# Optimization experiments

Measured on AMD Instinct MI355X. Metric: run time of the kernel, lower is better.

The kernel has to match this reference:

```python
import jax, jax.numpy as jnp
import numpy as np

L, B, DM, H, HID, NSPK, NB, NC, WIN = 128, 64, 1024, 256, 256, 2, 30, 6, 10
F = 2 * H            # biLSTM output feature dim
MEM = F + HID        # concat of node features and graph-conv output
R = 2 * NSPK * NSPK  # number of edge relations


def _build_edges():
    src_l, dst_l = [], []
    for j in range(L):
        for k in range(max(0, j - WIN), min(L, j + WIN + 1)):
            dst_l.append(j); src_l.append(k)
    dst = np.asarray(dst_l, np.int32); src = np.asarray(src_l, np.int32)
    offs = (np.arange(B, dtype=np.int32) * L)[:, None]
    edge_dst = (dst[None] + offs).reshape(-1)
    edge_src = (src[None] + offs).reshape(-1)
    mask = np.zeros((L, L), bool); mask[dst, src] = True
    return edge_src, edge_dst, mask


def setup_inputs():
    key = jax.random.key(0)
    ks = iter(jax.random.split(key, 32))
    rn = lambda *s: jax.random.normal(next(ks), s, jnp.float32) * 0.05
    edge_src, edge_dst, edge_mask = _build_edges()
    return {
        'U': jax.random.normal(next(ks), (L, B, DM), jnp.float32),
        'umask': jnp.ones((B, L), jnp.float32),
        'Wih0': rn(2, 4 * H, DM), 'Whh0': rn(2, 4 * H, H), 'b0': rn(2, 4 * H),
        'Wih1': rn(2, 4 * H, F), 'Whh1': rn(2, 4 * H, H), 'b1': rn(2, 4 * H),
        'W_scalar': rn(F, L),
        'basis': rn(NB, F, HID), 'comp': rn(R, NB),
        'W_root': rn(F, HID), 'b_rgcn': rn(HID),
        'gc_W1': rn(HID, HID), 'gc_W2': rn(HID, HID), 'gc_b': rn(HID),
        'Wm': rn(MEM, MEM), 'bm': rn(MEM),
        'Wl': rn(MEM, HID), 'bl': rn(HID),
        'Ws': rn(HID, NC), 'bs': rn(NC),
        'speakers': jax.random.randint(next(ks), (L, B), 0, NSPK, jnp.int32),
        'edge_src': jnp.asarray(edge_src), 'edge_dst': jnp.asarray(edge_dst),
        'edge_mask': jnp.asarray(edge_mask),
    }


def _lstm_dir(x, Wih, Whh, b, reverse):
    Bx, Hh = x.shape[1], Whh.shape[1]
    def step(carry, xt):
        h, c = carry
        g = xt @ Wih.T + h @ Whh.T + b          # PyTorch gate order i,f,g,o
        i, f, gg, o = jnp.split(g, 4, axis=-1)
        c = jax.nn.sigmoid(f) * c + jax.nn.sigmoid(i) * jnp.tanh(gg)
        h = jax.nn.sigmoid(o) * jnp.tanh(c)
        return (h, c), h
    init = (jnp.zeros((Bx, Hh), x.dtype), jnp.zeros((Bx, Hh), x.dtype))
    return jax.lax.scan(step, init, x, reverse=reverse)[1]


def _bilstm(x, Wih, Whh, b):
    return jnp.concatenate([_lstm_dir(x, Wih[0], Whh[0], b[0], False),
                            _lstm_dir(x, Wih[1], Whh[1], b[1], True)], -1)


def reference(U, umask, Wih0, Whh0, b0, Wih1, Whh1, b1, W_scalar, basis, comp,
              W_root, b_rgcn, gc_W1, gc_W2, gc_b, Wm, bm, Wl, bl, Ws, bs,
              speakers, edge_src, edge_dst, edge_mask):
    # --- 2-layer biLSTM encoder ---
    feats = _bilstm(_bilstm(U, Wih0, Whh0, b0), Wih1, Whh1, b1)   # (L,B,F)
    # --- MaskedEdgeAttention ('attn1'): edge weights ---
    scale = jnp.einsum('sbd,dm->sbm', feats, W_scalar)            # (L,B,L)
    alpha = jax.nn.softmax(scale, axis=0).transpose(1, 2, 0)      # (B,Lt,Ls)
    masked = alpha * jnp.where(edge_mask, 1.0, 1e-10)
    scores = masked / masked.sum(-1, keepdims=True) * edge_mask
    b_idx = edge_dst // L; i0 = edge_dst % L; i1 = edge_src % L
    edge_norm = scores[b_idx, i0, i1]                             # (E,)
    # --- edge types: speaker pair + temporal direction ---
    s_dst = speakers[i0, b_idx]; s_src = speakers[i1, b_idx]
    e_dir = jnp.where(i0 < i1, 0, 1)
    edge_type = s_dst * (2 * NSPK) + s_src * 2 + e_dir            # (E,) in [0,R)
    # --- node features, conversation-major ---
    x = feats.transpose(1, 0, 2).reshape(B * L, F)                # (N,F)
    N = B * L
    # --- RGCNConv with basis decomposition ---
    W_rel = jnp.einsum('rb,bfo->rfo', comp, basis)                # (R,F,HID)
    x_rel = jnp.einsum('nf,rfo->nro', x, W_rel)                   # (N,R,HID)
    msg = x_rel[edge_src, edge_type] * edge_norm[:, None]
    h = jax.ops.segment_sum(msg, edge_dst, num_segments=N) + x @ W_root + b_rgcn
    # --- GraphConv ---
    agg = jax.ops.segment_sum(h[edge_src], edge_dst, num_segments=N)
    h2 = h @ gc_W1 + gc_b + agg @ gc_W2                           # (N,HID)
    em = jnp.concatenate([x, h2], -1)                             # (N,MEM)
    em = em.reshape(B, L, MEM).transpose(1, 0, 2)                 # (L,B,MEM)
    # --- MatchingAttention ('general2') at every timestep, vectorized ---
    um = umask.T                                                  # (L,B)
    x_tr = em @ Wm + bm                                           # (L,B,MEM)
    logits = jnp.einsum('tbm,sbm->tbs', x_tr, em * um[:, :, None]) * umask[None]
    a = jax.nn.softmax(jnp.tanh(logits), axis=2) * umask[None]
    a = a / a.sum(2, keepdims=True)
    att = jnp.einsum('tbs,sbm->tbm', a, em)
    hidden = jax.nn.relu(att @ Wl + bl)                           # dropout = eval identity
    logp = jax.nn.log_softmax(hidden @ Ws + bs, axis=2)           # (L,B,NC)
    return logp.transpose(1, 0, 2).reshape(B * L, NC)
```

## Files before the change

### kernel.cpp

```cpp
#include <hip/hip_runtime.h>
#include <cstdint>


typedef __attribute__((ext_vector_type(8))) short bf16x8;
typedef __attribute__((ext_vector_type(4))) float f32x4;

template<bool HASBIAS, bool ACCUM, bool RELU, bool OUTBF>
__global__ __launch_bounds__(256) void gemm_bf16_nt(
    const ushort* __restrict__ A, const ushort* __restrict__ Bt,
    const float* __restrict__ bias, void* __restrict__ Cv,
    int M, int N, int K, long sA, long sB, long sC, long sBias)
{
  const int bz = blockIdx.z;
  A += (long)bz * sA;
  Bt += (long)bz * sB;
  if (HASBIAS) bias += (long)bz * sBias;
  float*  Cf = OUTBF ? nullptr : ((float*)Cv + (long)bz * sC);
  ushort* Cb = OUTBF ? ((ushort*)Cv + (long)bz * sC) : nullptr;

  const int bn = blockIdx.x * 128, bm = blockIdx.y * 128;

  __shared__ ushort As[128][40];
  __shared__ ushort Bs[128][40];

  const int tid = threadIdx.x;
  const int wave = tid >> 6, lane = tid & 63;
  const int wm = (wave >> 1) * 64, wn = (wave & 1) * 64;
  const int fr = lane & 15;
  const int fk = (lane >> 4) * 8;

  f32x4 acc[4][4];
#pragma unroll
  for (int i = 0; i < 4; ++i)
#pragma unroll
    for (int j = 0; j < 4; ++j) acc[i][j] = (f32x4){0.f, 0.f, 0.f, 0.f};

  const int sr = tid >> 1;
  const int sq = (tid & 1) * 16;

  for (int k0 = 0; k0 < K; k0 += 32) {
    const uint4* ga = (const uint4*)(A + (long)(bm + sr) * K + k0 + sq);
    uint4 av0 = ga[0], av1 = ga[1];
    const uint4* gb = (const uint4*)(Bt + (long)(bn + sr) * K + k0 + sq);
    uint4 bv0 = gb[0], bv1 = gb[1];
    *(uint4*)&As[sr][sq] = av0;
    *(uint4*)&As[sr][sq + 8] = av1;
    *(uint4*)&Bs[sr][sq] = bv0;
    *(uint4*)&Bs[sr][sq + 8] = bv1;
    __syncthreads();

    bf16x8 af[4], bfr[4];
#pragma unroll
    for (int f = 0; f < 4; ++f) {
      af[f]  = *(const bf16x8*)&As[wm + f * 16 + fr][fk];
      bfr[f] = *(const bf16x8*)&Bs[wn + f * 16 + fr][fk];
    }
#pragma unroll
    for (int mf = 0; mf < 4; ++mf)
#pragma unroll
      for (int nf = 0; nf < 4; ++nf)
        acc[mf][nf] = __builtin_amdgcn_mfma_f32_16x16x32_bf16(
            af[mf], bfr[nf], acc[mf][nf], 0, 0, 0);
    __syncthreads();
  }

  float bv[4];
#pragma unroll
  for (int nf = 0; nf < 4; ++nf)
    bv[nf] = HASBIAS ? bias[bn + wn + nf * 16 + fr] : 0.f;

  const int crow0 = (lane >> 4) * 4;
#pragma unroll
  for (int mf = 0; mf < 4; ++mf)
#pragma unroll
    for (int r = 0; r < 4; ++r) {
      const long roff = (long)(bm + wm + mf * 16 + crow0 + r) * N + bn + wn;
#pragma unroll
      for (int nf = 0; nf < 4; ++nf) {
        float v = acc[mf][nf][r] + bv[nf];
        if (OUTBF) {
          unsigned u = __float_as_uint(v);
          u += 0x7fffu + ((u >> 16) & 1u);
          Cb[roff + nf * 16 + fr] = (ushort)(u >> 16);
        } else {
          if (ACCUM) v += Cf[roff + nf * 16 + fr];
          if (RELU) v = fmaxf(v, 0.f);
          Cf[roff + nf * 16 + fr] = v;
        }
      }
    }
}

__device__ __forceinline__ unsigned short f2bf(float f) {
  unsigned u = __float_as_uint(f);
  u += 0x7fffu + ((u >> 16) & 1u);
  return (unsigned short)(u >> 16);
}
__device__ __forceinline__ float fast_sig(float x) {
  return __builtin_amdgcn_rcpf(1.f + __expf(-x));
}
__device__ __forceinline__ float fast_tanh(float x) {
  const float xc = fminf(fmaxf(x, -15.f), 15.f);
  const float t = __expf(2.f * xc);
  return (t - 1.f) * __builtin_amdgcn_rcpf(t + 1.f);
}

__device__ __forceinline__ int sdot4_(uint a, uint b, int c) {
#if __has_builtin(__builtin_amdgcn_sdot4)
  return __builtin_amdgcn_sdot4((int)a, (int)b, c, false);
#else
  int r = c;
  r += ((int)(a << 24) >> 24) * ((int)(b << 24) >> 24);
  r += ((int)(a << 16) >> 24) * ((int)(b << 16) >> 24);
  r += ((int)(a << 8)  >> 24) * ((int)(b << 8)  >> 24);
  r += ((int)a >> 24)         * ((int)b >> 24);
  return r;
#endif
}

__global__ __launch_bounds__(256) void cvt_bf16_k(const float* __restrict__ src,
                                                  ushort* __restrict__ dst) {
  const long i = ((long)blockIdx.x * 256 + threadIdx.x) * 4;
  float4 v = *(const float4*)(src + i);
  ushort4 o;
  o.x = f2bf(v.x); o.y = f2bf(v.y); o.z = f2bf(v.z); o.w = f2bf(v.w);
  *(ushort4*)(dst + i) = o;
}

__global__ __launch_bounds__(256) void tp_bf16_k(const float* __restrict__ src,
                                                 ushort* __restrict__ dst,
                                                 int R, int C) {
  __shared__ float tile[32][33];
  const int c0 = blockIdx.x * 32, r0 = blockIdx.y * 32;
  const int tx = threadIdx.x & 31, ty = threadIdx.x >> 5;
#pragma unroll
  for (int j = 0; j < 4; ++j)
    tile[ty + j * 8][tx] = src[(long)(r0 + ty + j * 8) * C + c0 + tx];
  __syncthreads();
#pragma unroll
  for (int j = 0; j < 4; ++j)
    dst[(long)(c0 + ty + j * 8) * R + r0 + tx] = f2bf(tile[tx][ty + j * 8]);
}

__global__ __launch_bounds__(256) void emt_k(const ushort* __restrict__ src,
                                             ushort* __restrict__ dst) {
  __shared__ ushort tile[32][33];
  const int c0 = blockIdx.x * 32;
  const int r0 = blockIdx.y * 32;
  const int b = blockIdx.z;
  const ushort* s = src + (long)b * 98304;
  ushort* d = dst + (long)b * 98304;
  const int tx = threadIdx.x & 31, ty = threadIdx.x >> 5;
#pragma unroll
  for (int j = 0; j < 4; ++j)
    tile[ty + j * 8][tx] = s[(long)(r0 + ty + j * 8) * 768 + c0 + tx];
  __syncthreads();
#pragma unroll
  for (int j = 0; j < 4; ++j)
    d[(long)(c0 + ty + j * 8) * 128 + r0 + tx] = tile[tx][ty + j * 8];
}

__global__ __launch_bounds__(256) void pack_whh_i8_k(const float* __restrict__ Whh,
                                                     uint* __restrict__ Wq,
                                                     float* __restrict__ fscale) {
  const int wid = (blockIdx.x * 256 + threadIdx.x) >> 6;
  const int lane = threadIdx.x & 63;
  const int d = wid >> 10, gi = wid & 1023;
  const float* row = Whh + ((long)d * 1024 + gi) * 256 + lane * 4;
  float v0 = row[0], v1 = row[1], v2 = row[2], v3 = row[3];
  float am = fmaxf(fmaxf(fabsf(v0), fabsf(v1)), fmaxf(fabsf(v2), fabsf(v3)));
#pragma unroll
  for (int off = 32; off > 0; off >>= 1) am = fmaxf(am, __shfl_xor(am, off, 64));
  am = fmaxf(am, 1e-12f);
  const float inv = 127.f / am;
  int q0 = __float2int_rn(v0 * inv), q1 = __float2int_rn(v1 * inv);
  int q2 = __float2int_rn(v2 * inv), q3 = __float2int_rn(v3 * inv);
  uint w = (uint)(q0 & 255) | ((uint)(q1 & 255) << 8) |
           ((uint)(q2 & 255) << 16) | ((uint)(q3 & 255) << 24);
  Wq[((long)d * 64 + lane) * 1024 + gi] = w;
  if (lane == 0) fscale[d * 1024 + gi] = am / 127.f;
}

__global__ __launch_bounds__(1024) void lstm4_k(
    const float* __restrict__ Xg,
    const uint* __restrict__ Wq,
    const float* __restrict__ fscale,
    ushort* __restrict__ out)
{
  const int bx = blockIdx.x;
  const int d = bx >> 6, b = bx & 63;
  const int tid = threadIdx.x;

  __shared__ uint hq[2][64];
  __shared__ float preactF[1024];

  uint w[64];
  const uint* wrow = Wq + (long)d * 65536 + tid;
#pragma unroll
  for (int k4 = 0; k4 < 64; ++k4) w[k4] = wrow[k4 * 1024];

  if (tid < 128) ((uint*)hq)[tid] = 0u;

  const float fsc = fscale[d * 1024 + tid] * (1.0f / 127.0f);
  const float* Xd = Xg + (long)d * 8192 * 1024;

  float c = 0.f;
  float x0 = 0.f, x1 = 0.f, x2 = 0.f, x3 = 0.f;
  if (tid < 256) {
    const float* xr = Xd + ((long)((d ? 127 : 0) * 64 + b)) * 1024;
    x0 = xr[tid]; x1 = xr[tid + 256]; x2 = xr[tid + 512]; x3 = xr[tid + 768];
  }
  __syncthreads();

  int cur = 0;
  for (int step = 0; step < 128; ++step) {
    const int t = d ? 127 - step : step;

    float n0 = 0.f, n1 = 0.f, n2 = 0.f, n3 = 0.f;
    if (tid < 256 && step + 1 < 128) {
      const float* xr = Xd + ((long)((d ? 126 - step : step + 1) * 64 + b)) * 1024;
      n0 = xr[tid]; n1 = xr[tid + 256]; n2 = xr[tid + 512]; n3 = xr[tid + 768];
    }

    int acc = 0;
    const uint4* hrow = (const uint4*)hq[cur];
#pragma unroll
    for (int k16 = 0; k16 < 16; ++k16) {
      uint4 h4 = hrow[k16];
      acc = sdot4_(w[k16 * 4 + 0], h4.x, acc);
      acc = sdot4_(w[k16 * 4 + 1], h4.y, acc);
      acc = sdot4_(w[k16 * 4 + 2], h4.z, acc);
      acc = sdot4_(w[k16 * 4 + 3], h4.w, acc);
    }
    preactF[tid] = (float)acc * fsc;
    __syncthreads();

    if (tid < 256) {
      float p0 = x0 + preactF[tid];
      float p1 = x1 + preactF[tid + 256];
      float p2 = x2 + preactF[tid + 512];
      float p3 = x3 + preactF[tid + 768];
      const float ig = fast_sig(p0), fg = fast_sig(p1);
      const float gg = fast_tanh(p2), og = fast_sig(p3);
      c = fg * c + ig * gg;
      const float h = og * fast_tanh(c);
      out[((long)(t * 64 + b)) * 512 + (d << 8) + tid] = f2bf(h);
      ((char*)hq[cur ^ 1])[tid] = (char)__float2int_rn(h * 127.f);
      x0 = n0; x1 = n1; x2 = n2; x3 = n3;
    }
    __syncthreads();
    cur ^= 1;
  }
}

__global__ __launch_bounds__(128) void edge_softmax_k(const float* __restrict__ scale,
                                                      float* __restrict__ scores) {
  const int bx = blockIdx.x;
  const int b = bx >> 7, t = bx & 127;
  const int s = threadIdx.x;
  __shared__ float red[128];
  const float v = scale[((long)(s * 64 + b)) * 128 + t];
  red[s] = v; __syncthreads();
  for (int off = 64; off > 0; off >>= 1) { if (s < off) red[s] = fmaxf(red[s], red[s + off]); __syncthreads(); }
  const float m = red[0]; __syncthreads();
  const float e = expf(v - m);
  red[s] = e; __syncthreads();
  for (int off = 64; off > 0; off >>= 1) { if (s < off) red[s] += red[s + off]; __syncthreads(); }
  const float esum = red[0]; __syncthreads();
  const float alpha = e / esum;
  const int dd = s - t;
  const bool inwin = (dd <= 10) && (dd >= -10);
  const float masked = alpha * (inwin ? 1.0f : 1e-10f);
  red[s] = masked; __syncthreads();
  for (int off = 64; off > 0; off >>= 1) { if (s < off) red[s] += red[s + off]; __syncthreads(); }
  const float msum = red[0];
  scores[(long)bx * 128 + s] = inwin ? (masked / msum) : 0.f;
}

__global__ __launch_bounds__(256) void xbuf_k(const ushort* __restrict__ featsbf,
                                              ushort* __restrict__ xbf) {
  const int n = blockIdx.x;
  const int b = n >> 7, t = n & 127;
  const int tid = threadIdx.x;
  const ushort* src = featsbf + (long)(t * 64 + b) * 512;
  ushort* dst = xbf + (long)n * 512;
  dst[tid] = src[tid];
  dst[tid + 256] = src[tid + 256];
}

__global__ __launch_bounds__(256) void wrel_k(const float* __restrict__ basis,
                                              const float* __restrict__ comp,
                                              ushort* __restrict__ wrel2t) {
  const int f = blockIdx.x;
  const int o = threadIdx.x;
  __shared__ float cs[240];
  if (o < 240) cs[o] = comp[o];
  __syncthreads();
  float acc[8];
#pragma unroll
  for (int r = 0; r < 8; ++r) acc[r] = 0.f;
  for (int bb = 0; bb < 30; ++bb) {
    const float v = basis[((long)bb * 512 + f) * 256 + o];
#pragma unroll
    for (int r = 0; r < 8; ++r) acc[r] = fmaf(cs[r * 30 + bb], v, acc[r]);
  }
#pragma unroll
  for (int r = 0; r < 8; ++r)
    wrel2t[((long)(r * 256 + o)) * 512 + f] = f2bf(acc[r]);
}

__global__ __launch_bounds__(256) void rgcn_gather_k(
    const float* __restrict__ xrel, const float* __restrict__ scores,
    const float* __restrict__ hroot, const int* __restrict__ spk,
    float* __restrict__ h, ushort* __restrict__ hbf)
{
  const int n = blockIdx.x;
  const int b = n >> 7, t = n & 127;
  const int o = threadIdx.x;
  const int lo = max(t - 10, 0), hi = min(t + 10, 127);
  const int cnt = hi - lo + 1;
  __shared__ int spks[21];
  __shared__ float wv[21];
  __shared__ int spkt_s;
  if (o < cnt) {
    spks[o] = spk[(lo + o) * 64 + b];
    wv[o] = scores[((long)(b * 128 + t)) * 128 + lo + o];
  }
  if (o == 0) spkt_s = spk[t * 64 + b];
  __syncthreads();
  const int spkt = spkt_s;
  float acc = hroot[(long)n * 256 + o];
  for (int q = 0; q < cnt; ++q) {
    const int s = lo + q;
    const int et = spkt * 4 + spks[q] * 2 + ((t < s) ? 0 : 1);
    acc = fmaf(xrel[(((long)(b * 128 + s)) * 8 + et) * 256 + o], wv[q], acc);
  }
  h[(long)n * 256 + o] = acc;
  hbf[(long)n * 256 + o] = f2bf(acc);
}

__global__ __launch_bounds__(256) void agg_k(const float* __restrict__ h,
                                             ushort* __restrict__ aggbf) {
  const int n = blockIdx.x;
  const int b = n >> 7, t = n & 127;
  const int o = threadIdx.x;
  const int lo = max(t - 10, 0), hi = min(t + 10, 127);
  float acc = 0.f;
  for (int s = lo; s <= hi; ++s) acc += h[((long)(b * 128 + s)) * 256 + o];
  aggbf[(long)n * 256 + o] = f2bf(acc);
}

__global__ __launch_bounds__(256) void em_k(const ushort* __restrict__ xbf,
                                            const float* __restrict__ h2,
                                            ushort* __restrict__ embf) {
  const int n = blockIdx.x;
  const int tid = threadIdx.x;
  embf[(long)n * 768 + tid] = xbf[(long)n * 512 + tid];
  embf[(long)n * 768 + 256 + tid] = xbf[(long)n * 512 + 256 + tid];
  embf[(long)n * 768 + 512 + tid] = f2bf(h2[(long)n * 256 + tid]);
}

__global__ __launch_bounds__(128) void match_softmax_k(const float* __restrict__ logits,
                                                       const float* __restrict__ umask,
                                                       ushort* __restrict__ abf) {
  const int bx = blockIdx.x;
  const int b = bx >> 7;
  const int s = threadIdx.x;
  __shared__ float red[128];
  const float* row = logits + (long)bx * 128;
  const float um = umask[b * 128 + s];
  const float v = tanhf(row[s] * um * um);
  red[s] = v; __syncthreads();
  for (int off = 64; off > 0; off >>= 1) { if (s < off) red[s] = fmaxf(red[s], red[s + off]); __syncthreads(); }
  const float m = red[0]; __syncthreads();
  const float e = expf(v - m);
  red[s] = e; __syncthreads();
  for (int off = 64; off > 0; off >>= 1) { if (s < off) red[s] += red[s + off]; __syncthreads(); }
  const float es = red[0]; __syncthreads();
  const float p = (e / es) * um;
  red[s] = p; __syncthreads();
  for (int off = 64; off > 0; off >>= 1) { if (s < off) red[s] += red[s + off]; __syncthreads(); }
  const float ps = red[0];
  abf[(long)bx * 128 + s] = f2bf(p / ps);
}

__global__ __launch_bounds__(256) void final_k(const float* __restrict__ hidden,
                                               const float* __restrict__ Ws,
                                               const float* __restrict__ bs,
                                               float* __restrict__ out) {
  __shared__ float wsl[256 * 6];
  const int tid = threadIdx.x;
#pragma unroll
  for (int j = 0; j < 6; ++j) wsl[tid * 6 + j] = Ws[tid * 6 + j];
  __syncthreads();
  const int wave = tid >> 6, lane = tid & 63;
  const int n = blockIdx.x * 4 + wave;
  const float4 hv = *(const float4*)&hidden[(long)n * 256 + lane * 4];
  const float hvv[4] = {hv.x, hv.y, hv.z, hv.w};
  float a[6];
#pragma unroll
  for (int c = 0; c < 6; ++c) a[c] = 0.f;
#pragma unroll
  for (int j = 0; j < 4; ++j)
#pragma unroll
    for (int c = 0; c < 6; ++c)
      a[c] = fmaf(hvv[j], wsl[(lane * 4 + j) * 6 + c], a[c]);
#pragma unroll
  for (int off = 32; off > 0; off >>= 1)
#pragma unroll
    for (int c = 0; c < 6; ++c)
      a[c] += __shfl_xor(a[c], off, 64);
  if (lane == 0) {
    float v[6], m = -1e30f;
#pragma unroll
    for (int c = 0; c < 6; ++c) { v[c] = a[c] + bs[c]; m = fmaxf(m, v[c]); }
    float sum = 0.f;
#pragma unroll
    for (int c = 0; c < 6; ++c) sum += expf(v[c] - m);
    const float lse = m + logf(sum);
#pragma unroll
    for (int c = 0; c < 6; ++c) out[(long)n * 6 + c] = v[c] - lse;
  }
}

extern "C" void kernel_launch(void* const* d_in, const int* in_sizes, int n_in,
                              void* d_out, int out_size, void* d_ws, size_t ws_size,
                              hipStream_t stream) {
  const float* U        = (const float*)d_in[0];
  const float* umask    = (const float*)d_in[1];
  const float* Wih0     = (const float*)d_in[2];
  const float* Whh0     = (const float*)d_in[3];
  const float* b0       = (const float*)d_in[4];
  const float* Wih1     = (const float*)d_in[5];
  const float* Whh1     = (const float*)d_in[6];
  const float* b1       = (const float*)d_in[7];
  const float* W_scalar = (const float*)d_in[8];
  const float* basis    = (const float*)d_in[9];
  const float* comp     = (const float*)d_in[10];
  const float* W_root   = (const float*)d_in[11];
  const float* b_rgcn   = (const float*)d_in[12];
  const float* gc_W1    = (const float*)d_in[13];
  const float* gc_W2    = (const float*)d_in[14];
  const float* gc_b     = (const float*)d_in[15];
  const float* Wm       = (const float*)d_in[16];
  const float* bm       = (const float*)d_in[17];
  const float* Wl       = (const float*)d_in[18];
  const float* bl       = (const float*)d_in[19];
  const float* Wsw      = (const float*)d_in[20];
  const float* bsw      = (const float*)d_in[21];
  const int*   speakers = (const int*)d_in[22];

  float* ws = (float*)d_ws;
  float* gates   = ws + 0L;
  float* feats   = ws + 16777216L;
  float* xbuf    = ws + 20971520L;
  float* feats0  = ws + 25165824L;
  float* scaleb  = ws + 29360128L;
  float* scoresb = ws + 30408704L;
  float* wrelr   = ws + 31457280L;
  float* hroot   = ws + 32505856L;
  uint*  wq      = (uint*)(ws + 34603008L);
  float* fsc     = ws + 34865152L;
  float* wTr     = ws + 34869248L;

  ushort* ubf    = (ushort*)xbuf;
  ushort* wih0bf = (ushort*)feats;
  ushort* wih1bf = (ushort*)(feats + 1048576L);
  ushort* featsbf= (ushort*)(feats + 2097152L);
  ushort* f0bf   = (ushort*)feats0;
  ushort* xbf    = (ushort*)xbuf;
  ushort* wrel2t = (ushort*)wrelr;
  ushort* wroott = (ushort*)wTr;
  ushort* gcW1t  = wroott + 131072L;
  ushort* gcW2t  = gcW1t + 65536L;
  ushort* Wmt    = gcW2t + 65536L;
  ushort* Wlt    = Wmt + 589824L;
  ushort* wscT   = (ushort*)scoresb;

  float*  hb      = feats0;
  ushort* hbf     = (ushort*)(feats0 + 2097152L);
  ushort* aggbf   = (ushort*)(feats0 + 3145728L);
  ushort* embf    = (ushort*)feats0;
  ushort* emT     = (ushort*)xbuf;
  ushort* xtrbf   = (ushort*)gates;
  ushort* abf     = (ushort*)scoresb;
  ushort* attbf   = (ushort*)feats;

  float*  xrel    = gates;
  float*  h2b     = hroot;
  float*  logitsb = scaleb;
  float*  hiddenb = scaleb;

  pack_whh_i8_k<<<512, 256, 0, stream>>>(Whh0, wq, fsc);
  pack_whh_i8_k<<<512, 256, 0, stream>>>(Whh1, wq + 131072, fsc + 2048);
  cvt_bf16_k<<<8192, 256, 0, stream>>>(U, ubf);
  cvt_bf16_k<<<2048, 256, 0, stream>>>(Wih0, wih0bf);
  cvt_bf16_k<<<1024, 256, 0, stream>>>(Wih1, wih1bf);
  tp_bf16_k<<<dim3(8, 16), 256, 0, stream>>>(W_root, wroott, 512, 256);
  tp_bf16_k<<<dim3(8, 8), 256, 0, stream>>>(gc_W1, gcW1t, 256, 256);
  tp_bf16_k<<<dim3(8, 8), 256, 0, stream>>>(gc_W2, gcW2t, 256, 256);
  tp_bf16_k<<<dim3(24, 24), 256, 0, stream>>>(Wm, Wmt, 768, 768);
  tp_bf16_k<<<dim3(8, 24), 256, 0, stream>>>(Wl, Wlt, 768, 256);
  tp_bf16_k<<<dim3(4, 16), 256, 0, stream>>>(W_scalar, wscT, 512, 128);
  wrel_k<<<512, 256, 0, stream>>>(basis, comp, wrel2t);

  gemm_bf16_nt<true, false, false, false><<<dim3(8, 64, 2), 256, 0, stream>>>(
      ubf, wih0bf, b0, gates, 8192, 1024, 1024, 0L, 1048576L, 8388608L, 1024L);
  lstm4_k<<<128, 1024, 0, stream>>>(gates, wq, fsc, f0bf);

  gemm_bf16_nt<true, false, false, false><<<dim3(8, 64, 2), 256, 0, stream>>>(
      f0bf, wih1bf, b1, gates, 8192, 1024, 512, 0L, 524288L, 8388608L, 1024L);
  lstm4_k<<<128, 1024, 0, stream>>>(gates, wq + 131072, fsc + 2048, featsbf);

  gemm_bf16_nt<false, false, false, false><<<dim3(1, 64, 1), 256, 0, stream>>>(
      featsbf, wscT, nullptr, scaleb, 8192, 128, 512, 0L, 0L, 0L, 0L);
  edge_softmax_k<<<8192, 128, 0, stream>>>(scaleb, scoresb);

  xbuf_k<<<8192, 256, 0, stream>>>(featsbf, xbf);
  gemm_bf16_nt<true, false, false, false><<<dim3(2, 64, 1), 256, 0, stream>>>(
      xbf, wroott, b_rgcn, hroot, 8192, 256, 512, 0L, 0L, 0L, 0L);
  gemm_bf16_nt<false, false, false, false><<<dim3(16, 64, 1), 256, 0, stream>>>(
      xbf, wrel2t, nullptr, xrel, 8192, 2048, 512, 0L, 0L, 0L, 0L);
  rgcn_gather_k<<<8192, 256, 0, stream>>>(xrel, scoresb, hroot, speakers, hb, hbf);

  agg_k<<<8192, 256, 0, stream>>>(hb, aggbf);
  gemm_bf16_nt<true, false, false, false><<<dim3(2, 64, 1), 256, 0, stream>>>(
      hbf, gcW1t, gc_b, h2b, 8192, 256, 256, 0L, 0L, 0L, 0L);
  gemm_bf16_nt<false, true, false, false><<<dim3(2, 64, 1), 256, 0, stream>>>(
      aggbf, gcW2t, nullptr, h2b, 8192, 256, 256, 0L, 0L, 0L, 0L);

  em_k<<<8192, 256, 0, stream>>>(xbf, h2b, embf);
  gemm_bf16_nt<true, false, false, true><<<dim3(6, 64, 1), 256, 0, stream>>>(
      embf, Wmt, bm, xtrbf, 8192, 768, 768, 0L, 0L, 0L, 0L);
  emt_k<<<dim3(24, 4, 64), 256, 0, stream>>>(embf, emT);
  gemm_bf16_nt<false, false, false, false><<<dim3(1, 1, 64), 256, 0, stream>>>(
      xtrbf, embf, nullptr, logitsb, 128, 128, 768, 98304L, 98304L, 16384L, 0L);
  match_softmax_k<<<8192, 128, 0, stream>>>(logitsb, umask, abf);
  gemm_bf16_nt<false, false, false, true><<<dim3(6, 1, 64), 256, 0, stream>>>(
      abf, emT, nullptr, attbf, 128, 768, 128, 16384L, 98304L, 98304L, 0L);

  gemm_bf16_nt<true, false, true, false><<<dim3(2, 64, 1), 256, 0, stream>>>(
      attbf, Wlt, bl, hiddenb, 8192, 256, 768, 0L, 0L, 0L, 0L);
  final_k<<<2048, 256, 0, stream>>>(hiddenb, Wsw, bsw, (float*)d_out);
}
```

Measured before the change: 676.0 us.

## Split LSTM recurrent dot over k-slices and reduce with shuffles, dropping a barrier

The int8 recurrent weights are repacked so each thread holds all four gates of one hidden unit over a quarter of the K dimension. Partial sums are combined with wave shuffles, so the shared preactivation buffer and one __syncthreads per timestep go away. tanh is rewritten in terms of the existing sigmoid helper. The trade is extra shuffle work, and only one lane in four doing the gate math, in exchange for one less block barrier on the serial 128-step critical path.

```diff
diff --git a/kernel.cpp b/kernel.cpp
--- a/kernel.cpp
+++ b/kernel.cpp
@@ -100,9 +100,7 @@
   return __builtin_amdgcn_rcpf(1.f + __expf(-x));
 }
 __device__ __forceinline__ float fast_tanh(float x) {
-  const float xc = fminf(fmaxf(x, -15.f), 15.f);
-  const float t = __expf(2.f * xc);
-  return (t - 1.f) * __builtin_amdgcn_rcpf(t + 1.f);
+  return 2.f * fast_sig(2.f * x) - 1.f;
 }
 
 __device__ __forceinline__ int sdot4_(uint a, uint b, int c) {
@@ -166,6 +164,7 @@
   const int wid = (blockIdx.x * 256 + threadIdx.x) >> 6;
   const int lane = threadIdx.x & 63;
   const int d = wid >> 10, gi = wid & 1023;
+  const int g = gi >> 8, i = gi & 255;
   const float* row = Whh + ((long)d * 1024 + gi) * 256 + lane * 4;
   float v0 = row[0], v1 = row[1], v2 = row[2], v3 = row[3];
   float am = fmaxf(fmaxf(fabsf(v0), fabsf(v1)), fmaxf(fabsf(v2), fabsf(v3)));
@@ -177,11 +176,13 @@
   int q2 = __float2int_rn(v2 * inv), q3 = __float2int_rn(v3 * inv);
   uint w = (uint)(q0 & 255) | ((uint)(q1 & 255) << 8) |
            ((uint)(q2 & 255) << 16) | ((uint)(q3 & 255) << 24);
-  Wq[((long)d * 64 + lane) * 1024 + gi] = w;
+  const int j = lane & 15, ks = lane >> 4;
+  const int t = (i >> 4) * 64 + (i & 15) * 4 + ks;
+  Wq[(long)(((d * 16 + j) * 4 + g)) * 1024 + t] = w;
   if (lane == 0) fscale[d * 1024 + gi] = am / 127.f;
 }
 
-__global__ __launch_bounds__(1024) void lstm4_k(
+__global__ __launch_bounds__(1024) void lstm5_k(
     const float* __restrict__ Xg,
     const uint* __restrict__ Wq,
     const float* __restrict__ fscale,
@@ -190,25 +191,41 @@
   const int bx = blockIdx.x;
   const int d = bx >> 6, b = bx & 63;
   const int tid = threadIdx.x;
+  const int lane = tid & 63;
+  const int ks = lane & 3;
+  const int i = (tid >> 6) * 16 + (lane >> 2);
+  const bool fin = (ks == 0);
 
   __shared__ uint hq[2][64];
-  __shared__ float preactF[1024];
 
   uint w[64];
-  const uint* wrow = Wq + (long)d * 65536 + tid;
-#pragma unroll
-  for (int k4 = 0; k4 < 64; ++k4) w[k4] = wrow[k4 * 1024];
+  {
+    const uint* wb = Wq + (long)d * 65536 + tid;
+#pragma unroll
+    for (int j = 0; j < 16; ++j)
+#pragma unroll
+      for (int g = 0; g < 4; ++g)
+        w[j * 4 + g] = wb[(j * 4 + g) * 1024];
+  }
 
   if (tid < 128) ((uint*)hq)[tid] = 0u;
 
-  const float fsc = fscale[d * 1024 + tid] * (1.0f / 127.0f);
+  float fsc0 = 0.f, fsc1 = 0.f, fsc2 = 0.f, fsc3 = 0.f;
+  if (fin) {
+    const float* fs = fscale + d * 1024 + i;
+    fsc0 = fs[0] * (1.f / 127.f);
+    fsc1 = fs[256] * (1.f / 127.f);
+    fsc2 = fs[512] * (1.f / 127.f);
+    fsc3 = fs[768] * (1.f / 127.f);
+  }
+
   const float* Xd = Xg + (long)d * 8192 * 1024;
 
   float c = 0.f;
   float x0 = 0.f, x1 = 0.f, x2 = 0.f, x3 = 0.f;
-  if (tid < 256) {
-    const float* xr = Xd + ((long)((d ? 127 : 0) * 64 + b)) * 1024;
-    x0 = xr[tid]; x1 = xr[tid + 256]; x2 = xr[tid + 512]; x3 = xr[tid + 768];
+  if (fin) {
+    const float* xr = Xd + ((long)((d ? 127 : 0) * 64 + b)) * 1024 + i;
+    x0 = xr[0]; x1 = xr[256]; x2 = xr[512]; x3 = xr[768];
   }
   __syncthreads();
 
@@ -217,35 +234,49 @@
     const int t = d ? 127 - step : step;
 
     float n0 = 0.f, n1 = 0.f, n2 = 0.f, n3 = 0.f;
-    if (tid < 256 && step + 1 < 128) {
-      const float* xr = Xd + ((long)((d ? 126 - step : step + 1) * 64 + b)) * 1024;
-      n0 = xr[tid]; n1 = xr[tid + 256]; n2 = xr[tid + 512]; n3 = xr[tid + 768];
+    if (fin && step + 1 < 128) {
+      const float* xr = Xd + ((long)((d ? 126 - step : step + 1) * 64 + b)) * 1024 + i;
+      n0 = xr[0]; n1 = xr[256]; n2 = xr[512]; n3 = xr[768];
     }
 
-    int acc = 0;
-    const uint4* hrow = (const uint4*)hq[cur];
-#pragma unroll
-    for (int k16 = 0; k16 < 16; ++k16) {
-      uint4 h4 = hrow[k16];
-      acc = sdot4_(w[k16 * 4 + 0], h4.x, acc);
-      acc = sdot4_(w[k16 * 4 + 1], h4.y, acc);
-      acc = sdot4_(w[k16 * 4 + 2], h4.z, acc);
-      acc = sdot4_(w[k16 * 4 + 3], h4.w, acc);
+    int a0 = 0, a1 = 0, a2 = 0, a3 = 0;
+    const uint4* hrow4 = (const uint4*)hq[cur];
+#pragma unroll
+    for (int jj = 0; jj < 4; ++jj) {
+      uint4 h4 = hrow4[ks * 4 + jj];
+      a0 = sdot4_(w[(jj * 4 + 0) * 4 + 0], h4.x, a0);
+      a1 = sdot4_(w[(jj * 4 + 0) * 4 + 1], h4.x, a1);
+      a2 = sdot4_(w[(jj * 4 + 0) * 4 + 2], h4.x, a2);
+      a3 = sdot4_(w[(jj * 4 + 0) * 4 + 3], h4.x, a3);
+      a0 = sdot4_(w[(jj * 4 + 1) * 4 + 0], h4.y, a0);
+      a1 = sdot4_(w[(jj * 4 + 1) * 4 + 1], h4.y, a1);
+      a2 = sdot4_(w[(jj * 4 + 1) * 4 + 2], h4.y, a2);
+      a3 = sdot4_(w[(jj * 4 + 1) * 4 + 3], h4.y, a3);
+      a0 = sdot4_(w[(jj * 4 + 2) * 4 + 0], h4.z, a0);
+      a1 = sdot4_(w[(jj * 4 + 2) * 4 + 1], h4.z, a1);
+      a2 = sdot4_(w[(jj * 4 + 2) * 4 + 2], h4.z, a2);
+      a3 = sdot4_(w[(jj * 4 + 2) * 4 + 3], h4.z, a3);
+      a0 = sdot4_(w[(jj * 4 + 3) * 4 + 0], h4.w, a0);
+      a1 = sdot4_(w[(jj * 4 + 3) * 4 + 1], h4.w, a1);
+      a2 = sdot4_(w[(jj * 4 + 3) * 4 + 2], h4.w, a2);
+      a3 = sdot4_(w[(jj * 4 + 3) * 4 + 3], h4.w, a3);
     }
-    preactF[tid] = (float)acc * fsc;
-    __syncthreads();
-
-    if (tid < 256) {
-      float p0 = x0 + preactF[tid];
-      float p1 = x1 + preactF[tid + 256];
-      float p2 = x2 + preactF[tid + 512];
-      float p3 = x3 + preactF[tid + 768];
+    a0 += __shfl_xor(a0, 1, 64); a0 += __shfl_xor(a0, 2, 64);
+    a1 += __shfl_xor(a1, 1, 64); a1 += __shfl_xor(a1, 2, 64);
+    a2 += __shfl_xor(a2, 1, 64); a2 += __shfl_xor(a2, 2, 64);
+    a3 += __shfl_xor(a3, 1, 64); a3 += __shfl_xor(a3, 2, 64);
+
+    if (fin) {
+      const float p0 = x0 + (float)a0 * fsc0;
+      const float p1 = x1 + (float)a1 * fsc1;
+      const float p2 = x2 + (float)a2 * fsc2;
+      const float p3 = x3 + (float)a3 * fsc3;
       const float ig = fast_sig(p0), fg = fast_sig(p1);
       const float gg = fast_tanh(p2), og = fast_sig(p3);
       c = fg * c + ig * gg;
       const float h = og * fast_tanh(c);
-      out[((long)(t * 64 + b)) * 512 + (d << 8) + tid] = f2bf(h);
-      ((char*)hq[cur ^ 1])[tid] = (char)__float2int_rn(h * 127.f);
+      out[((long)(t * 64 + b)) * 512 + (d << 8) + i] = f2bf(h);
+      ((char*)hq[cur ^ 1])[i] = (char)__float2int_rn(h * 127.f);
       x0 = n0; x1 = n1; x2 = n2; x3 = n3;
     }
     __syncthreads();
@@ -506,11 +537,11 @@
 
   gemm_bf16_nt<true, false, false, false><<<dim3(8, 64, 2), 256, 0, stream>>>(
       ubf, wih0bf, b0, gates, 8192, 1024, 1024, 0L, 1048576L, 8388608L, 1024L);
-  lstm4_k<<<128, 1024, 0, stream>>>(gates, wq, fsc, f0bf);
+  lstm5_k<<<128, 1024, 0, stream>>>(gates, wq, fsc, f0bf);
 
   gemm_bf16_nt<true, false, false, false><<<dim3(8, 64, 2), 256, 0, stream>>>(
       f0bf, wih1bf, b1, gates, 8192, 1024, 512, 0L, 524288L, 8388608L, 1024L);
-  lstm4_k<<<128, 1024, 0, stream>>>(gates, wq + 131072, fsc + 2048, featsbf);
+  lstm5_k<<<128, 1024, 0, stream>>>(gates, wq + 131072, fsc + 2048, featsbf);
 
   gemm_bf16_nt<false, false, false, false><<<dim3(1, 64, 1), 256, 0, stream>>>(
       featsbf, wscT, nullptr, scaleb, 8192, 128, 512, 0L, 0L, 0L, 0L);
```

After: 784.9 us. 16.1% more time.

## Compute all four LSTM gates per thread to drop the preactivation barrier

Applied to the files above, without the earlier changes.

The recurrent LSTM kernel now runs 256 threads per block instead of 1024. Each thread owns one hidden unit and computes all four gate dot products over int8 weights held in 256 registers. This removes the shared-memory preactivation buffer and one __syncthreads per timestep, and the int8 weight packing is reordered to match. It also rewrites tanh as 2*sigmoid(2x)-1. The risks are heavy register pressure that could spill, and 4x more serial sdot4 work per thread.

```diff
diff --git a/kernel.cpp b/kernel.cpp
--- a/kernel.cpp
+++ b/kernel.cpp
@@ -100,9 +100,7 @@
   return __builtin_amdgcn_rcpf(1.f + __expf(-x));
 }
 __device__ __forceinline__ float fast_tanh(float x) {
-  const float xc = fminf(fmaxf(x, -15.f), 15.f);
-  const float t = __expf(2.f * xc);
-  return (t - 1.f) * __builtin_amdgcn_rcpf(t + 1.f);
+  return 2.f * fast_sig(2.f * x) - 1.f;
 }
 
 __device__ __forceinline__ int sdot4_(uint a, uint b, int c) {
@@ -166,6 +164,7 @@
   const int wid = (blockIdx.x * 256 + threadIdx.x) >> 6;
   const int lane = threadIdx.x & 63;
   const int d = wid >> 10, gi = wid & 1023;
+  const int g = gi >> 8, i = gi & 255;
   const float* row = Whh + ((long)d * 1024 + gi) * 256 + lane * 4;
   float v0 = row[0], v1 = row[1], v2 = row[2], v3 = row[3];
   float am = fmaxf(fmaxf(fabsf(v0), fabsf(v1)), fmaxf(fabsf(v2), fabsf(v3)));
@@ -177,11 +176,11 @@
   int q2 = __float2int_rn(v2 * inv), q3 = __float2int_rn(v3 * inv);
   uint w = (uint)(q0 & 255) | ((uint)(q1 & 255) << 8) |
            ((uint)(q2 & 255) << 16) | ((uint)(q3 & 255) << 24);
-  Wq[((long)d * 64 + lane) * 1024 + gi] = w;
+  Wq[(long)(((d * 64 + lane) * 4 + g)) * 256 + i] = w;
   if (lane == 0) fscale[d * 1024 + gi] = am / 127.f;
 }
 
-__global__ __launch_bounds__(1024) void lstm4_k(
+__global__ __launch_bounds__(256, 1) void lstm6_k(
     const float* __restrict__ Xg,
     const uint* __restrict__ Wq,
     const float* __restrict__ fscale,
@@ -189,26 +188,32 @@
 {
   const int bx = blockIdx.x;
   const int d = bx >> 6, b = bx & 63;
-  const int tid = threadIdx.x;
+  const int i = threadIdx.x;
 
   __shared__ uint hq[2][64];
-  __shared__ float preactF[1024];
-
-  uint w[64];
-  const uint* wrow = Wq + (long)d * 65536 + tid;
-#pragma unroll
-  for (int k4 = 0; k4 < 64; ++k4) w[k4] = wrow[k4 * 1024];
-
-  if (tid < 128) ((uint*)hq)[tid] = 0u;
-
-  const float fsc = fscale[d * 1024 + tid] * (1.0f / 127.0f);
+
+  uint w[256];
+  {
+    const uint* wb = Wq + (long)d * 65536 + i;
+#pragma unroll
+    for (int q = 0; q < 256; ++q) w[q] = wb[q * 256];
+  }
+
+  if (i < 64) hq[0][i] = 0u;
+
+  const float* fs = fscale + d * 1024 + i;
+  const float fsc0 = fs[0] * (1.f / 127.f);
+  const float fsc1 = fs[256] * (1.f / 127.f);
+  const float fsc2 = fs[512] * (1.f / 127.f);
+  const float fsc3 = fs[768] * (1.f / 127.f);
+
   const float* Xd = Xg + (long)d * 8192 * 1024;
 
   float c = 0.f;
-  float x0 = 0.f, x1 = 0.f, x2 = 0.f, x3 = 0.f;
-  if (tid < 256) {
-    const float* xr = Xd + ((long)((d ? 127 : 0) * 64 + b)) * 1024;
-    x0 = xr[tid]; x1 = xr[tid + 256]; x2 = xr[tid + 512]; x3 = xr[tid + 768];
+  float x0, x1, x2, x3;
+  {
+    const float* xr = Xd + ((long)((d ? 127 : 0) * 64 + b)) * 1024 + i;
+    x0 = xr[0]; x1 = xr[256]; x2 = xr[512]; x3 = xr[768];
   }
   __syncthreads();
 
@@ -217,37 +222,45 @@
     const int t = d ? 127 - step : step;
 
     float n0 = 0.f, n1 = 0.f, n2 = 0.f, n3 = 0.f;
-    if (tid < 256 && step + 1 < 128) {
-      const float* xr = Xd + ((long)((d ? 126 - step : step + 1) * 64 + b)) * 1024;
-      n0 = xr[tid]; n1 = xr[tid + 256]; n2 = xr[tid + 512]; n3 = xr[tid + 768];
+    if (step + 1 < 128) {
+      const float* xr = Xd + ((long)((d ? 126 - step : step + 1) * 64 + b)) * 1024 + i;
+      n0 = xr[0]; n1 = xr[256]; n2 = xr[512]; n3 = xr[768];
     }
 
-    int acc = 0;
-    const uint4* hrow = (const uint4*)hq[cur];
+    int a0 = 0, a1 = 0, a2 = 0, a3 = 0;
+    const uint4* h4p = (const uint4*)hq[cur];
 #pragma unroll
     for (int k16 = 0; k16 < 16; ++k16) {
-      uint4 h4 = hrow[k16];
-      acc = sdot4_(w[k16 * 4 + 0], h4.x, acc);
-      acc = sdot4_(w[k16 * 4 + 1], h4.y, acc);
-      acc = sdot4_(w[k16 * 4 + 2], h4.z, acc);
-      acc = sdot4_(w[k16 * 4 + 3], h4.w, acc);
+      uint4 h4 = h4p[k16];
+      a0 = sdot4_(w[(k16 * 4 + 0) * 4 + 0], h4.x, a0);
+      a1 = sdot4_(w[(k16 * 4 + 0) * 4 + 1], h4.x, a1);
+      a2 = sdot4_(w[(k16 * 4 + 0) * 4 + 2], h4.x, a2);
+      a3 = sdot4_(w[(k16 * 4 + 0) * 4 + 3], h4.x, a3);
+      a0 = sdot4_(w[(k16 * 4 + 1) * 4 + 0], h4.y, a0);
+      a1 = sdot4_(w[(k16 * 4 + 1) * 4 + 1], h4.y, a1);
+      a2 = sdot4_(w[(k16 * 4 + 1) * 4 + 2], h4.y, a2);
+      a3 = sdot4_(w[(k16 * 4 + 1) * 4 + 3], h4.y, a3);
+      a0 = sdot4_(w[(k16 * 4 + 2) * 4 + 0], h4.z, a0);
+      a1 = sdot4_(w[(k16 * 4 + 2) * 4 + 1], h4.z, a1);
+      a2 = sdot4_(w[(k16 * 4 + 2) * 4 + 2], h4.z, a2);
+      a3 = sdot4_(w[(k16 * 4 + 2) * 4 + 3], h4.z, a3);
+      a0 = sdot4_(w[(k16 * 4 + 3) * 4 + 0], h4.w, a0);
+      a1 = sdot4_(w[(k16 * 4 + 3) * 4 + 1], h4.w, a1);
+      a2 = sdot4_(w[(k16 * 4 + 3) * 4 + 2], h4.w, a2);
+      a3 = sdot4_(w[(k16 * 4 + 3) * 4 + 3], h4.w, a3);
     }
-    preactF[tid] = (float)acc * fsc;
-    __syncthreads();
-
-    if (tid < 256) {
-      float p0 = x0 + preactF[tid];
-      float p1 = x1 + preactF[tid + 256];
-      float p2 = x2 + preactF[tid + 512];
-      float p3 = x3 + preactF[tid + 768];
-      const float ig = fast_sig(p0), fg = fast_sig(p1);
-      const float gg = fast_tanh(p2), og = fast_sig(p3);
-      c = fg * c + ig * gg;
-      const float h = og * fast_tanh(c);
-      out[((long)(t * 64 + b)) * 512 + (d << 8) + tid] = f2bf(h);
-      ((char*)hq[cur ^ 1])[tid] = (char)__float2int_rn(h * 127.f);
-      x0 = n0; x1 = n1; x2 = n2; x3 = n3;
-    }
+
+    const float p0 = x0 + (float)a0 * fsc0;
+    const float p1 = x1 + (float)a1 * fsc1;
+    const float p2 = x2 + (float)a2 * fsc2;
+    const float p3 = x3 + (float)a3 * fsc3;
+    const float ig = fast_sig(p0), fg = fast_sig(p1);
+    const float gg = fast_tanh(p2), og = fast_sig(p3);
+    c = fg * c + ig * gg;
+    const float h = og * fast_tanh(c);
+    out[((long)(t * 64 + b)) * 512 + (d << 8) + i] = f2bf(h);
+    ((char*)hq[cur ^ 1])[i] = (char)__float2int_rn(h * 127.f);
+    x0 = n0; x1 = n1; x2 = n2; x3 = n3;
     __syncthreads();
     cur ^= 1;
   }
@@ -506,11 +519,11 @@
 
   gemm_bf16_nt<true, false, false, false><<<dim3(8, 64, 2), 256, 0, stream>>>(
       ubf, wih0bf, b0, gates, 8192, 1024, 1024, 0L, 1048576L, 8388608L, 1024L);
-  lstm4_k<<<128, 1024, 0, stream>>>(gates, wq, fsc, f0bf);
+  lstm6_k<<<128, 256, 0, stream>>>(gates, wq, fsc, f0bf);
 
   gemm_bf16_nt<true, false, false, false><<<dim3(8, 64, 2), 256, 0, stream>>>(
       f0bf, wih1bf, b1, gates, 8192, 1024, 512, 0L, 524288L, 8388608L, 1024L);
-  lstm4_k<<<128, 1024, 0, stream>>>(gates, wq + 131072, fsc + 2048, featsbf);
+  lstm6_k<<<128, 256, 0, stream>>>(gates, wq + 131072, fsc + 2048, featsbf);
 
   gemm_bf16_nt<false, false, false, false><<<dim3(1, 64, 1), 256, 0, stream>>>(
       featsbf, wscT, nullptr, scaleb, 8192, 128, 512, 0L, 0L, 0L, 0L);
```

New measurement: 847.0 us. 1.25x slower.
